# Kernel tuning notes

Hardware: AMD Instinct MI355X
Metric: run time of the kernel (lower is better)

Reference implementation:

```python
import jax, jax.numpy as jnp
import numpy as np

DEPTH = 8  # binary soft-decision-tree depth (n_node = 2**DEPTH - 1, n_leaf = 2**DEPTH)


def setup_inputs() -> dict:
    key = jax.random.key(0)
    k0, k1, k2 = jax.random.split(key, 3)
    B, T, D = 32, 2048, 512
    K, L = 8, 16  # n_trees, n_label
    n_node = 2 ** DEPTH - 1
    n_leaf = 2 ** DEPTH
    x = jax.random.normal(k0, (B, T, D), dtype=jnp.float32)
    W = jax.random.normal(k1, (K, n_node, D), dtype=jnp.float32) * (1.0 / np.sqrt(D))
    b = jnp.zeros((K, n_node), dtype=jnp.float32)
    pi = jax.random.uniform(k2, (K, n_leaf, L), dtype=jnp.float32)
    return {"x": x, "W": W, "b": b, "pi": pi, "conditional": 1, "dependence_length": -1}


def _tree_preds(x, W, b, pi):
    # decision probs for all trees at once: [K, B, T, n_node]
    d = jax.nn.sigmoid(jnp.einsum('btf,knf->kbtn', x, W) + b[:, None, None, :])
    mu = jnp.ones(d.shape[:3] + (1,), dtype=d.dtype)  # routing prob, [K,B,T,1]
    begin = 0
    for layer in range(DEPTH):
        w = 2 ** layer
        dl = d[..., begin:begin + w]  # [K,B,T,w]
        # interleave (mu*d, mu*(1-d)) -> children order matches torch repeat/cat flatten
        mu = jnp.stack([mu * dl, mu * (1.0 - dl)], axis=-1).reshape(d.shape[:3] + (2 * w,))
        begin += w
    # leaf distributions: softmax over labels of pi, then mix by routing probs
    return jnp.einsum('kbtl,kln->kbtn', mu, jax.nn.softmax(pi, axis=-1))  # [K,B,T,L]


def reference(x, W, b, pi, conditional, dependence_length):
    K = W.shape[0]
    L = pi.shape[-1]
    B, T, _ = x.shape
    tp = _tree_preds(x, W, b, pi)  # [K,B,T,L]
    if not conditional:
        return tp.sum(0) * (1.0 / L)
    if dependence_length == -1:
        tp_t = jnp.transpose(tp, (2, 1, 0, 3))  # [T,B,K,L] for token scan
        init = jnp.full((B, L), 1.0 / L, dtype=x.dtype)
        def step(tmp, tpt):
            tmp = jax.lax.stop_gradient(tmp)  # mirrors clone().detach()
            new = jnp.einsum('bkl,bk->bl', tpt, tmp[:, :K])
            return jax.nn.softmax(jnp.exp(new), axis=1), new
        _, preds = jax.lax.scan(step, init, tp_t)  # preds: [T,B,L]
        return jnp.transpose(preds, (1, 0, 2))
    # dependence_length >= 1 path
    pred = tp.sum(0) / K
    pad = jnp.full((B, 1, L), 1.0 / L, dtype=x.dtype)
    for _ in range(1, dependence_length):
        shifted = jnp.concatenate([pad, pred[:, :-1, :]], axis=1)
        pred = jnp.einsum('kbtl,btk->btl', tp, shifted[:, :, :K])
    return pred
```

## Files before the change

### kernel.cpp

```cpp
#include <hip/hip_runtime.h>

#define KT 8
#define NN 255
#define LL 16
#define DD 512
#define BB 32
#define TT 2048
#define MM (BB*TT)

typedef short short8 __attribute__((ext_vector_type(8)));
typedef float floatx4 __attribute__((ext_vector_type(4)));

__device__ __forceinline__ unsigned bf16_rne(float v) {
    unsigned u = __float_as_uint(v);
    return (u + 0x7FFFu + ((u >> 16) & 1u)) >> 16;
}

__device__ __forceinline__ void gll16(const char* g, char* l) {
    __builtin_amdgcn_global_load_lds(
        (const __attribute__((address_space(1))) unsigned int*)g,
        (__attribute__((address_space(3))) unsigned int*)l, 16, 0, 0);
}

__global__ void k_prep_x(const float* __restrict__ x, short* __restrict__ xh,
                         short* __restrict__ xl) {
    size_t g = (size_t)blockIdx.x * 256 + threadIdx.x;
    const float4* xv = (const float4*)x;
    float4 a = xv[g * 2], b = xv[g * 2 + 1];
    float v[8] = {a.x, a.y, a.z, a.w, b.x, b.y, b.z, b.w};
    short8 hh, ll;
    #pragma unroll
    for (int j = 0; j < 8; ++j) {
        unsigned h = bf16_rne(v[j]);
        hh[j] = (short)h;
        ll[j] = (short)bf16_rne(v[j] - __uint_as_float(h << 16));
    }
    ((short8*)xh)[g] = hh;
    ((short8*)xl)[g] = ll;
}

__global__ void k_prep_sp(const float* __restrict__ pi, float* __restrict__ spd) {
    int g = blockIdx.x * blockDim.x + threadIdx.x;
    const float* p = pi + (size_t)g * LL;
    float v[LL];
    float mx = -1e30f;
    #pragma unroll
    for (int l = 0; l < LL; ++l) { v[l] = p[l]; mx = fmaxf(mx, v[l]); }
    float s = 0.f;
    #pragma unroll
    for (int l = 0; l < LL; ++l) { v[l] = __expf(v[l] - mx); s += v[l]; }
    const float inv = 1.0f / s;
    float* o = spd + (size_t)g * LL;
    #pragma unroll
    for (int l = 0; l < LL; ++l) o[l] = v[l] * inv;
}

__global__ void k_prep_b(const float* __restrict__ W, short* __restrict__ Bp) {
    int g = blockIdx.x * 256 + threadIdx.x;
    int lane = g & 63;
    int nt = (g >> 6) & 15;
    int kb = (g >> 10) & 15;
    int kt = g >> 14;
    int n = nt * 16 + (lane & 15);
    int k0 = kb * 32 + ((lane >> 4) << 3);
    short8 hh = {0,0,0,0,0,0,0,0}, ll = {0,0,0,0,0,0,0,0};
    if (n < NN) {
        const float* wp = W + ((size_t)kt * NN + n) * DD + k0;
        floatx4 a = *(const floatx4*)wp;
        floatx4 b = *(const floatx4*)(wp + 4);
        float xv[8] = {a[0], a[1], a[2], a[3], b[0], b[1], b[2], b[3]};
        #pragma unroll
        for (int j = 0; j < 8; ++j) {
            unsigned h = bf16_rne(xv[j]);
            hh[j] = (short)h;
            ll[j] = (short)bf16_rne(xv[j] - __uint_as_float(h << 16));
        }
    }
    size_t base = ((((size_t)kt * 16 + kb) * 16 + nt) * 2) * 64;
    ((short8*)Bp)[base + lane] = hh;
    ((short8*)Bp)[base + 64 + lane] = ll;
}

__global__ void k_prep_spf(const float* __restrict__ spd, short* __restrict__ spf) {
    int g = blockIdx.x * 64 + threadIdx.x;
    int lane = g & 63;
    int ks = (g >> 6) & 7;
    int kt = g >> 9;
    int n = lane & 15;
    int oct = lane >> 4;
    short8 hh, ll;
    #pragma unroll
    for (int j = 0; j < 8; ++j) {
        int leaf = ks * 32 + oct * 8 + j;
        float v = spd[((size_t)kt * 256 + leaf) * 16 + n];
        unsigned h = bf16_rne(v);
        hh[j] = (short)h;
        ll[j] = (short)bf16_rne(v - __uint_as_float(h << 16));
    }
    size_t base = ((size_t)(kt * 8 + ks) * 2) * 64;
    ((short8*)spf)[base + lane] = hh;
    ((short8*)spf)[base + 64 + lane] = ll;
}

__launch_bounds__(512, 2)
__global__ void k_forest(const short* __restrict__ xh, const short* __restrict__ xl,
                         const short* __restrict__ Bp, const float* __restrict__ bias,
                         const short* __restrict__ spf, float* __restrict__ tp) {
    __shared__ __align__(16) char smem[65536];
    const int tid  = threadIdx.x;
    const int lane = tid & 63;
    const int wv   = tid >> 6;
    const int wr   = wv >> 1;
    const int wc   = wv & 1;
    const int kt   = blockIdx.x;
    const int mb   = blockIdx.y;
    const int oct  = lane >> 4;

    const int mrow0 = mb * 128 + wr * 32;
    const short* xhb = xh + (size_t)(mrow0 + (lane & 15)) * DD + (oct << 3);
    const short* xlb = xl + (size_t)(mrow0 + (lane & 15)) * DD + (oct << 3);
    const char* bsrc = (const char*)Bp + (size_t)kt * 16 * 32768;

    float breg[8];
    #pragma unroll
    for (int ntl = 0; ntl < 8; ++ntl) {
        int n = wc * 128 + ntl * 16 + (lane & 15);
        breg[ntl] = (n < NN) ? bias[kt * NN + n] : 0.f;
    }

    floatx4 acc[2][8];
    #pragma unroll
    for (int mt = 0; mt < 2; ++mt)
        #pragma unroll
        for (int ntl = 0; ntl < 8; ++ntl)
            acc[mt][ntl] = (floatx4){0.f, 0.f, 0.f, 0.f};

    short8 ahc[2], alc[2], ahn[2], aln[2];

    #pragma unroll
    for (int i = 0; i < 4; ++i)
        gll16(bsrc + i * 8192 + tid * 16, (char*)smem + i * 8192 + tid * 16);
    #pragma unroll
    for (int mt = 0; mt < 2; ++mt) {
        ahc[mt] = *(const short8*)(xhb + (size_t)mt * 16 * DD);
        alc[mt] = *(const short8*)(xlb + (size_t)mt * 16 * DD);
    }
    __syncthreads();

    #pragma unroll 2
    for (int kb = 0; kb < 16; ++kb) {
        char* cur = (char*)smem + ((kb & 1) ? 32768 : 0);
        char* nxt = (char*)smem + ((kb & 1) ? 0 : 32768);
        if (kb < 15) {
            const char* s = bsrc + (size_t)(kb + 1) * 32768;
            #pragma unroll
            for (int i = 0; i < 4; ++i)
                gll16(s + i * 8192 + tid * 16, nxt + i * 8192 + tid * 16);
            #pragma unroll
            for (int mt = 0; mt < 2; ++mt) {
                ahn[mt] = *(const short8*)(xhb + (size_t)mt * 16 * DD + (kb + 1) * 32);
                aln[mt] = *(const short8*)(xlb + (size_t)mt * 16 * DD + (kb + 1) * 32);
            }
        }
        const short8* bf = (const short8*)cur;
        #pragma unroll
        for (int ntl = 0; ntl < 8; ++ntl) {
            const int nt = wc * 8 + ntl;
            short8 bh = bf[(size_t)(nt * 2 + 0) * 64 + lane];
            short8 bl = bf[(size_t)(nt * 2 + 1) * 64 + lane];
            #pragma unroll
            for (int mt = 0; mt < 2; ++mt) {
                acc[mt][ntl] = __builtin_amdgcn_mfma_f32_16x16x32_bf16(ahc[mt], bh, acc[mt][ntl], 0, 0, 0);
                acc[mt][ntl] = __builtin_amdgcn_mfma_f32_16x16x32_bf16(ahc[mt], bl, acc[mt][ntl], 0, 0, 0);
                acc[mt][ntl] = __builtin_amdgcn_mfma_f32_16x16x32_bf16(alc[mt], bh, acc[mt][ntl], 0, 0, 0);
            }
        }
        __syncthreads();
        #pragma unroll
        for (int mt = 0; mt < 2; ++mt) {
            ahc[mt] = ahn[mt]; alc[mt] = aln[mt];
        }
    }

    float* dls = (float*)smem;
    const short8* spl = (const short8*)((char*)smem + 33280);
    floatx4* ps = (floatx4*)((char*)smem + 49664);

    {
        const floatx4* src = (const floatx4*)(spf + (size_t)kt * 8192);
        floatx4* dst = (floatx4*)((char*)smem + 33280);
        dst[tid] = src[tid];
        dst[512 + tid] = src[512 + tid];
    }

    const int mtile = wv & 1;
    const int wg = wv >> 1;
    const int mloc = mtile * 16 + (lane & 15);

    #pragma unroll 1
    for (int p = 0; p < 4; ++p) {
        __syncthreads();
        if (wr == p) {
            #pragma unroll
            for (int mt = 0; mt < 2; ++mt)
                #pragma unroll
                for (int ntl = 0; ntl < 8; ++ntl)
                    #pragma unroll
                    for (int i = 0; i < 4; ++i) {
                        float lg = acc[mt][ntl][i] + breg[ntl];
                        float dv = 1.f / (1.f + __expf(-lg));
                        int mrow = mt * 16 + oct * 4 + i;
                        int n = wc * 128 + ntl * 16 + (lane & 15);
                        dls[mrow * 260 + n] = dv;
                    }
        }
        __syncthreads();

        const float* dm = dls + mloc * 260;
        floatx4 pacc = (floatx4){0.f, 0.f, 0.f, 0.f};
        #pragma unroll
        for (int kss = 0; kss < 2; ++kss) {
            const int ks = wg * 2 + kss;
            const int leaf0 = ks * 32 + oct * 8;
            float d0 = dm[0];
            float d1 = dm[1 + (leaf0 >> 7)];
            float d2 = dm[3 + (leaf0 >> 6)];
            float d3 = dm[7 + (leaf0 >> 5)];
            float d4 = dm[15 + (leaf0 >> 4)];
            float d5 = dm[31 + (leaf0 >> 3)];
            float n6a = dm[63 + (leaf0 >> 2)];
            float n6b = dm[64 + (leaf0 >> 2)];
            float v70 = dm[127 + (leaf0 >> 1)];
            float v71 = dm[128 + (leaf0 >> 1)];
            float v72 = dm[129 + (leaf0 >> 1)];
            float v73 = dm[130 + (leaf0 >> 1)];
            float P = (((leaf0 >> 7) & 1) ? (1.f - d0) : d0)
                    * (((leaf0 >> 6) & 1) ? (1.f - d1) : d1)
                    * (((leaf0 >> 5) & 1) ? (1.f - d2) : d2)
                    * (((leaf0 >> 4) & 1) ? (1.f - d3) : d3)
                    * (((leaf0 >> 3) & 1) ? (1.f - d4) : d4);
            float pA = P * d5, pB = P * (1.f - d5);
            float q0 = pA * n6a, q1 = pA * (1.f - n6a);
            float q2 = pB * n6b, q3 = pB * (1.f - n6b);
            float mu[8];
            mu[0] = q0 * v70; mu[1] = q0 * (1.f - v70);
            mu[2] = q1 * v71; mu[3] = q1 * (1.f - v71);
            mu[4] = q2 * v72; mu[5] = q2 * (1.f - v72);
            mu[6] = q3 * v73; mu[7] = q3 * (1.f - v73);
            short8 mh, ml;
            #pragma unroll
            for (int j = 0; j < 8; ++j) {
                unsigned h = bf16_rne(mu[j]);
                mh[j] = (short)h;
                ml[j] = (short)bf16_rne(mu[j] - __uint_as_float(h << 16));
            }
            short8 sh = spl[(ks * 2 + 0) * 64 + lane];
            short8 sl = spl[(ks * 2 + 1) * 64 + lane];
            pacc = __builtin_amdgcn_mfma_f32_16x16x32_bf16(mh, sh, pacc, 0, 0, 0);
            pacc = __builtin_amdgcn_mfma_f32_16x16x32_bf16(mh, sl, pacc, 0, 0, 0);
            pacc = __builtin_amdgcn_mfma_f32_16x16x32_bf16(ml, sh, pacc, 0, 0, 0);
        }
        ps[(mtile * 4 + wg) * 64 + lane] = pacc;
        __syncthreads();
        if (wv < 2) {
            const int mt2 = wv;
            floatx4 r = ps[(mt2 * 4 + 0) * 64 + lane] + ps[(mt2 * 4 + 1) * 64 + lane]
                      + ps[(mt2 * 4 + 2) * 64 + lane] + ps[(mt2 * 4 + 3) * 64 + lane];
            #pragma unroll
            for (int i = 0; i < 4; ++i) {
                size_t mg = (size_t)mb * 128 + p * 32 + mt2 * 16 + oct * 4 + i;
                tp[mg * 128 + kt * 16 + (lane & 15)] = r[i];
            }
        }
    }
}

__device__ __forceinline__ float dpp_sum16(float v) {
    int i;
    i = __builtin_amdgcn_update_dpp(0, __float_as_int(v), 0xB1, 0xF, 0xF, true);
    v += __int_as_float(i);
    i = __builtin_amdgcn_update_dpp(0, __float_as_int(v), 0x4E, 0xF, 0xF, true);
    v += __int_as_float(i);
    i = __builtin_amdgcn_update_dpp(0, __float_as_int(v), 0x141, 0xF, 0xF, true);
    v += __int_as_float(i);
    i = __builtin_amdgcn_update_dpp(0, __float_as_int(v), 0x140, 0xF, 0xF, true);
    v += __int_as_float(i);
    return v;
}

__device__ __forceinline__ float rdl(float v, int k) {
    return __int_as_float(__builtin_amdgcn_readlane(__float_as_int(v), k));
}

#define SCAN_STEP(C, t) do { \
    float nw = ((C[0]*w0 + C[1]*w1) + (C[2]*w2 + C[3]*w3)) \
             + ((C[4]*w4 + C[5]*w5) + (C[6]*w6 + C[7]*w7)); \
    nw *= rinv; \
    ob[(size_t)(t) * 16] = nw; \
    float e1 = __expf(nw); \
    float wx = __expf(e1); \
    if ((t) + 8 < TT) { \
        _Pragma("unroll") \
        for (int k = 0; k < 8; ++k) C[k] = base[(size_t)((t) + 8) * 128 + k * 16]; \
    } \
    float ssum = dpp_sum16(wx); \
    rinv = __builtin_amdgcn_rcpf(ssum); \
    w0 = rdl(wx, 0); w1 = rdl(wx, 1); w2 = rdl(wx, 2); w3 = rdl(wx, 3); \
    w4 = rdl(wx, 4); w5 = rdl(wx, 5); w6 = rdl(wx, 6); w7 = rdl(wx, 7); \
} while (0)

__global__ void k_scan(const float* __restrict__ tp, float* __restrict__ out) {
    const int b = blockIdx.x;
    const int l = threadIdx.x;
    if (l >= 16) return;
    const float* base = tp + (size_t)b * TT * 128 + l;
    float* ob = out + (size_t)b * TT * 16 + l;
    float w0 = 1.f, w1 = 1.f, w2 = 1.f, w3 = 1.f, w4 = 1.f, w5 = 1.f, w6 = 1.f, w7 = 1.f;
    float rinv = 1.f / 16.f;
    float c0[8], c1[8], c2[8], c3[8], c4[8], c5[8], c6[8], c7[8];
    #pragma unroll
    for (int k = 0; k < 8; ++k) {
        c0[k] = base[(size_t)0 * 128 + k * 16];
        c1[k] = base[(size_t)1 * 128 + k * 16];
        c2[k] = base[(size_t)2 * 128 + k * 16];
        c3[k] = base[(size_t)3 * 128 + k * 16];
        c4[k] = base[(size_t)4 * 128 + k * 16];
        c5[k] = base[(size_t)5 * 128 + k * 16];
        c6[k] = base[(size_t)6 * 128 + k * 16];
        c7[k] = base[(size_t)7 * 128 + k * 16];
    }
    for (int t0 = 0; t0 < TT; t0 += 8) {
        SCAN_STEP(c0, t0 + 0);
        SCAN_STEP(c1, t0 + 1);
        SCAN_STEP(c2, t0 + 2);
        SCAN_STEP(c3, t0 + 3);
        SCAN_STEP(c4, t0 + 4);
        SCAN_STEP(c5, t0 + 5);
        SCAN_STEP(c6, t0 + 6);
        SCAN_STEP(c7, t0 + 7);
    }
}

extern "C" void kernel_launch(void* const* d_in, const int* in_sizes, int n_in,
                              void* d_out, int out_size, void* d_ws, size_t ws_size,
                              hipStream_t stream) {
    const float* x  = (const float*)d_in[0];
    const float* W  = (const float*)d_in[1];
    const float* b  = (const float*)d_in[2];
    const float* pi = (const float*)d_in[3];
    float* ws = (float*)d_ws;
    float* tp  = ws;
    short* xh  = (short*)(ws + 8388608);
    short* xl  = xh + 33554432;
    short* Bp  = xl + 33554432;
    short* spf = Bp + 2097152;
    float* spd = (float*)(spf + 65536);
    float* out = (float*)d_out;

    k_prep_x<<<dim3(16384), dim3(256), 0, stream>>>(x, xh, xl);
    k_prep_sp<<<dim3(8), dim3(256), 0, stream>>>(pi, spd);
    k_prep_b<<<dim3(512), dim3(256), 0, stream>>>(W, Bp);
    k_prep_spf<<<dim3(64), dim3(64), 0, stream>>>(spd, spf);
    k_forest<<<dim3(8, 512), dim3(512), 0, stream>>>(xh, xl, Bp, b, spf, tp);
    k_scan<<<dim3(BB), dim3(64), 0, stream>>>(tp, out);
}
```

Before: 1.300 ms.

## Retile forest GEMM waves, transpose scan input layout, fuse leaf-softmax prep kernels

Several changes land together. The forest GEMM switches its wave grid from 4x2 to 2x4, so each wave owns a 64x64 tile and reuses each B fragment across four M tiles instead of two. The tree-prediction buffer is stored label-major with trees contiguous, padded per batch, so the serial scan reads each step with two float4 loads instead of eight strided scalar loads. The scan also normalises the weights before broadcasting them and drops the tail guard by relying on the padding. The two softmax/bf16-split prep kernels are merged into one that uses shared memory, removing a launch and an intermediate buffer. The larger accumulator footprint raises register pressure.

```diff
diff --git a/kernel.cpp b/kernel.cpp
--- a/kernel.cpp
+++ b/kernel.cpp
@@ -7,6 +7,7 @@
 #define BB 32
 #define TT 2048
 #define MM (BB*TT)
+#define TPS_STRIDE (2056*128)
 
 typedef short short8 __attribute__((ext_vector_type(8)));
 typedef float floatx4 __attribute__((ext_vector_type(4)));
@@ -39,9 +40,11 @@
     ((short8*)xl)[g] = ll;
 }
 
-__global__ void k_prep_sp(const float* __restrict__ pi, float* __restrict__ spd) {
-    int g = blockIdx.x * blockDim.x + threadIdx.x;
-    const float* p = pi + (size_t)g * LL;
+__global__ void k_prep_sp(const float* __restrict__ pi, short* __restrict__ spf) {
+    __shared__ float sm[256 * 16];
+    const int kt = blockIdx.x;
+    const int tid = threadIdx.x;
+    const float* p = pi + ((size_t)kt * 256 + tid) * LL;
     float v[LL];
     float mx = -1e30f;
     #pragma unroll
@@ -50,9 +53,27 @@
     #pragma unroll
     for (int l = 0; l < LL; ++l) { v[l] = __expf(v[l] - mx); s += v[l]; }
     const float inv = 1.0f / s;
-    float* o = spd + (size_t)g * LL;
-    #pragma unroll
-    for (int l = 0; l < LL; ++l) o[l] = v[l] * inv;
+    #pragma unroll
+    for (int l = 0; l < LL; ++l) sm[tid * 16 + l] = v[l] * inv;
+    __syncthreads();
+    #pragma unroll
+    for (int it = 0; it < 2; ++it) {
+        int item = it * 256 + tid;
+        int ks = item >> 6, lane = item & 63;
+        int n = lane & 15, oct = lane >> 4;
+        short8 hh, ll;
+        #pragma unroll
+        for (int j = 0; j < 8; ++j) {
+            int leaf = ks * 32 + oct * 8 + j;
+            float val = sm[leaf * 16 + n];
+            unsigned h = bf16_rne(val);
+            hh[j] = (short)h;
+            ll[j] = (short)bf16_rne(val - __uint_as_float(h << 16));
+        }
+        size_t base = ((size_t)(kt * 8 + ks) * 2) * 64;
+        ((short8*)spf)[base + lane] = hh;
+        ((short8*)spf)[base + 64 + lane] = ll;
+    }
 }
 
 __global__ void k_prep_b(const float* __restrict__ W, short* __restrict__ Bp) {
@@ -81,67 +102,46 @@
     ((short8*)Bp)[base + 64 + lane] = ll;
 }
 
-__global__ void k_prep_spf(const float* __restrict__ spd, short* __restrict__ spf) {
-    int g = blockIdx.x * 64 + threadIdx.x;
-    int lane = g & 63;
-    int ks = (g >> 6) & 7;
-    int kt = g >> 9;
-    int n = lane & 15;
-    int oct = lane >> 4;
-    short8 hh, ll;
-    #pragma unroll
-    for (int j = 0; j < 8; ++j) {
-        int leaf = ks * 32 + oct * 8 + j;
-        float v = spd[((size_t)kt * 256 + leaf) * 16 + n];
-        unsigned h = bf16_rne(v);
-        hh[j] = (short)h;
-        ll[j] = (short)bf16_rne(v - __uint_as_float(h << 16));
-    }
-    size_t base = ((size_t)(kt * 8 + ks) * 2) * 64;
-    ((short8*)spf)[base + lane] = hh;
-    ((short8*)spf)[base + 64 + lane] = ll;
-}
-
 __launch_bounds__(512, 2)
 __global__ void k_forest(const short* __restrict__ xh, const short* __restrict__ xl,
                          const short* __restrict__ Bp, const float* __restrict__ bias,
-                         const short* __restrict__ spf, float* __restrict__ tp) {
+                         const short* __restrict__ spf, float* __restrict__ tps) {
     __shared__ __align__(16) char smem[65536];
     const int tid  = threadIdx.x;
     const int lane = tid & 63;
     const int wv   = tid >> 6;
-    const int wr   = wv >> 1;
-    const int wc   = wv & 1;
+    const int wr   = wv >> 2;
+    const int wc   = wv & 3;
     const int kt   = blockIdx.x;
     const int mb   = blockIdx.y;
     const int oct  = lane >> 4;
-
-    const int mrow0 = mb * 128 + wr * 32;
-    const short* xhb = xh + (size_t)(mrow0 + (lane & 15)) * DD + (oct << 3);
-    const short* xlb = xl + (size_t)(mrow0 + (lane & 15)) * DD + (oct << 3);
+    const int lr   = lane & 15;
+
+    const short* xhb = xh + (size_t)(mb * 128 + wr * 64 + lr) * DD + (oct << 3);
+    const short* xlb = xl + (size_t)(mb * 128 + wr * 64 + lr) * DD + (oct << 3);
     const char* bsrc = (const char*)Bp + (size_t)kt * 16 * 32768;
 
-    float breg[8];
-    #pragma unroll
-    for (int ntl = 0; ntl < 8; ++ntl) {
-        int n = wc * 128 + ntl * 16 + (lane & 15);
+    float breg[4];
+    #pragma unroll
+    for (int ntl = 0; ntl < 4; ++ntl) {
+        int n = (wc * 4 + ntl) * 16 + lr;
         breg[ntl] = (n < NN) ? bias[kt * NN + n] : 0.f;
     }
 
-    floatx4 acc[2][8];
-    #pragma unroll
-    for (int mt = 0; mt < 2; ++mt)
-        #pragma unroll
-        for (int ntl = 0; ntl < 8; ++ntl)
+    floatx4 acc[4][4];
+    #pragma unroll
+    for (int mt = 0; mt < 4; ++mt)
+        #pragma unroll
+        for (int ntl = 0; ntl < 4; ++ntl)
             acc[mt][ntl] = (floatx4){0.f, 0.f, 0.f, 0.f};
 
-    short8 ahc[2], alc[2], ahn[2], aln[2];
+    short8 ahc[4], alc[4], ahn[4], aln[4];
 
     #pragma unroll
     for (int i = 0; i < 4; ++i)
         gll16(bsrc + i * 8192 + tid * 16, (char*)smem + i * 8192 + tid * 16);
     #pragma unroll
-    for (int mt = 0; mt < 2; ++mt) {
+    for (int mt = 0; mt < 4; ++mt) {
         ahc[mt] = *(const short8*)(xhb + (size_t)mt * 16 * DD);
         alc[mt] = *(const short8*)(xlb + (size_t)mt * 16 * DD);
     }
@@ -157,19 +157,19 @@
             for (int i = 0; i < 4; ++i)
                 gll16(s + i * 8192 + tid * 16, nxt + i * 8192 + tid * 16);
             #pragma unroll
-            for (int mt = 0; mt < 2; ++mt) {
+            for (int mt = 0; mt < 4; ++mt) {
                 ahn[mt] = *(const short8*)(xhb + (size_t)mt * 16 * DD + (kb + 1) * 32);
                 aln[mt] = *(const short8*)(xlb + (size_t)mt * 16 * DD + (kb + 1) * 32);
             }
         }
         const short8* bf = (const short8*)cur;
         #pragma unroll
-        for (int ntl = 0; ntl < 8; ++ntl) {
-            const int nt = wc * 8 + ntl;
+        for (int ntl = 0; ntl < 4; ++ntl) {
+            const int nt = wc * 4 + ntl;
             short8 bh = bf[(size_t)(nt * 2 + 0) * 64 + lane];
             short8 bl = bf[(size_t)(nt * 2 + 1) * 64 + lane];
             #pragma unroll
-            for (int mt = 0; mt < 2; ++mt) {
+            for (int mt = 0; mt < 4; ++mt) {
                 acc[mt][ntl] = __builtin_amdgcn_mfma_f32_16x16x32_bf16(ahc[mt], bh, acc[mt][ntl], 0, 0, 0);
                 acc[mt][ntl] = __builtin_amdgcn_mfma_f32_16x16x32_bf16(ahc[mt], bl, acc[mt][ntl], 0, 0, 0);
                 acc[mt][ntl] = __builtin_amdgcn_mfma_f32_16x16x32_bf16(alc[mt], bh, acc[mt][ntl], 0, 0, 0);
@@ -177,7 +177,7 @@
         }
         __syncthreads();
         #pragma unroll
-        for (int mt = 0; mt < 2; ++mt) {
+        for (int mt = 0; mt < 4; ++mt) {
             ahc[mt] = ahn[mt]; alc[mt] = aln[mt];
         }
     }
@@ -195,22 +195,23 @@
 
     const int mtile = wv & 1;
     const int wg = wv >> 1;
-    const int mloc = mtile * 16 + (lane & 15);
+    const int mloc = mtile * 16 + lr;
 
     #pragma unroll 1
     for (int p = 0; p < 4; ++p) {
         __syncthreads();
-        if (wr == p) {
-            #pragma unroll
-            for (int mt = 0; mt < 2; ++mt)
+        if (wr == (p >> 1)) {
+            const int mts = (p & 1) * 2;
+            #pragma unroll
+            for (int mtl = 0; mtl < 2; ++mtl)
                 #pragma unroll
-                for (int ntl = 0; ntl < 8; ++ntl)
+                for (int ntl = 0; ntl < 4; ++ntl)
                     #pragma unroll
                     for (int i = 0; i < 4; ++i) {
-                        float lg = acc[mt][ntl][i] + breg[ntl];
+                        float lg = acc[mts + mtl][ntl][i] + breg[ntl];
                         float dv = 1.f / (1.f + __expf(-lg));
-                        int mrow = mt * 16 + oct * 4 + i;
-                        int n = wc * 128 + ntl * 16 + (lane & 15);
+                        int mrow = mtl * 16 + oct * 4 + i;
+                        int n = (wc * 4 + ntl) * 16 + lr;
                         dls[mrow * 260 + n] = dv;
                     }
         }
@@ -268,8 +269,9 @@
                       + ps[(mt2 * 4 + 2) * 64 + lane] + ps[(mt2 * 4 + 3) * 64 + lane];
             #pragma unroll
             for (int i = 0; i < 4; ++i) {
-                size_t mg = (size_t)mb * 128 + p * 32 + mt2 * 16 + oct * 4 + i;
-                tp[mg * 128 + kt * 16 + (lane & 15)] = r[i];
+                int mg = mb * 128 + p * 32 + mt2 * 16 + oct * 4 + i;
+                int bb_ = mg >> 11, t = mg & 2047;
+                tps[(size_t)bb_ * TPS_STRIDE + (size_t)t * 128 + lr * 8 + kt] = r[i];
             }
         }
     }
@@ -292,52 +294,46 @@
     return __int_as_float(__builtin_amdgcn_readlane(__float_as_int(v), k));
 }
 
-#define SCAN_STEP(C, t) do { \
-    float nw = ((C[0]*w0 + C[1]*w1) + (C[2]*w2 + C[3]*w3)) \
-             + ((C[4]*w4 + C[5]*w5) + (C[6]*w6 + C[7]*w7)); \
-    nw *= rinv; \
+#define SCAN_STEP(CA, CB, t) do { \
+    float nw = ((CA[0]*w0 + CA[1]*w1) + (CA[2]*w2 + CA[3]*w3)) \
+             + ((CB[0]*w4 + CB[1]*w5) + (CB[2]*w6 + CB[3]*w7)); \
     ob[(size_t)(t) * 16] = nw; \
-    float e1 = __expf(nw); \
-    float wx = __expf(e1); \
-    if ((t) + 8 < TT) { \
-        _Pragma("unroll") \
-        for (int k = 0; k < 8; ++k) C[k] = base[(size_t)((t) + 8) * 128 + k * 16]; \
-    } \
+    float wx = __expf(__expf(nw)); \
+    CA = *(const floatx4*)(base + (size_t)((t) + 8) * 128); \
+    CB = *(const floatx4*)(base + (size_t)((t) + 8) * 128 + 4); \
     float ssum = dpp_sum16(wx); \
-    rinv = __builtin_amdgcn_rcpf(ssum); \
-    w0 = rdl(wx, 0); w1 = rdl(wx, 1); w2 = rdl(wx, 2); w3 = rdl(wx, 3); \
-    w4 = rdl(wx, 4); w5 = rdl(wx, 5); w6 = rdl(wx, 6); w7 = rdl(wx, 7); \
+    float wn = wx * __builtin_amdgcn_rcpf(ssum); \
+    w0 = rdl(wn, 0); w1 = rdl(wn, 1); w2 = rdl(wn, 2); w3 = rdl(wn, 3); \
+    w4 = rdl(wn, 4); w5 = rdl(wn, 5); w6 = rdl(wn, 6); w7 = rdl(wn, 7); \
 } while (0)
 
-__global__ void k_scan(const float* __restrict__ tp, float* __restrict__ out) {
+__global__ void k_scan(const float* __restrict__ tps, float* __restrict__ out) {
     const int b = blockIdx.x;
     const int l = threadIdx.x;
     if (l >= 16) return;
-    const float* base = tp + (size_t)b * TT * 128 + l;
+    const float* base = tps + (size_t)b * TPS_STRIDE + l * 8;
     float* ob = out + (size_t)b * TT * 16 + l;
-    float w0 = 1.f, w1 = 1.f, w2 = 1.f, w3 = 1.f, w4 = 1.f, w5 = 1.f, w6 = 1.f, w7 = 1.f;
-    float rinv = 1.f / 16.f;
-    float c0[8], c1[8], c2[8], c3[8], c4[8], c5[8], c6[8], c7[8];
-    #pragma unroll
-    for (int k = 0; k < 8; ++k) {
-        c0[k] = base[(size_t)0 * 128 + k * 16];
-        c1[k] = base[(size_t)1 * 128 + k * 16];
-        c2[k] = base[(size_t)2 * 128 + k * 16];
-        c3[k] = base[(size_t)3 * 128 + k * 16];
-        c4[k] = base[(size_t)4 * 128 + k * 16];
-        c5[k] = base[(size_t)5 * 128 + k * 16];
-        c6[k] = base[(size_t)6 * 128 + k * 16];
-        c7[k] = base[(size_t)7 * 128 + k * 16];
-    }
+    float w0 = 1.f/16.f, w1 = 1.f/16.f, w2 = 1.f/16.f, w3 = 1.f/16.f;
+    float w4 = 1.f/16.f, w5 = 1.f/16.f, w6 = 1.f/16.f, w7 = 1.f/16.f;
+    floatx4 a0, a1, a2, a3, a4, a5, a6, a7;
+    floatx4 b0, b1, b2, b3, b4, b5, b6, b7;
+    a0 = *(const floatx4*)(base + 0*128); b0 = *(const floatx4*)(base + 0*128 + 4);
+    a1 = *(const floatx4*)(base + 1*128); b1 = *(const floatx4*)(base + 1*128 + 4);
+    a2 = *(const floatx4*)(base + 2*128); b2 = *(const floatx4*)(base + 2*128 + 4);
+    a3 = *(const floatx4*)(base + 3*128); b3 = *(const floatx4*)(base + 3*128 + 4);
+    a4 = *(const floatx4*)(base + 4*128); b4 = *(const floatx4*)(base + 4*128 + 4);
+    a5 = *(const floatx4*)(base + 5*128); b5 = *(const floatx4*)(base + 5*128 + 4);
+    a6 = *(const floatx4*)(base + 6*128); b6 = *(const floatx4*)(base + 6*128 + 4);
+    a7 = *(const floatx4*)(base + 7*128); b7 = *(const floatx4*)(base + 7*128 + 4);
     for (int t0 = 0; t0 < TT; t0 += 8) {
-        SCAN_STEP(c0, t0 + 0);
-        SCAN_STEP(c1, t0 + 1);
-        SCAN_STEP(c2, t0 + 2);
-        SCAN_STEP(c3, t0 + 3);
-        SCAN_STEP(c4, t0 + 4);
-        SCAN_STEP(c5, t0 + 5);
-        SCAN_STEP(c6, t0 + 6);
-        SCAN_STEP(c7, t0 + 7);
+        SCAN_STEP(a0, b0, t0 + 0);
+        SCAN_STEP(a1, b1, t0 + 1);
+        SCAN_STEP(a2, b2, t0 + 2);
+        SCAN_STEP(a3, b3, t0 + 3);
+        SCAN_STEP(a4, b4, t0 + 4);
+        SCAN_STEP(a5, b5, t0 + 5);
+        SCAN_STEP(a6, b6, t0 + 6);
+        SCAN_STEP(a7, b7, t0 + 7);
     }
 }
 
@@ -349,18 +345,16 @@
     const float* b  = (const float*)d_in[2];
     const float* pi = (const float*)d_in[3];
     float* ws = (float*)d_ws;
-    float* tp  = ws;
-    short* xh  = (short*)(ws + 8388608);
+    float* tps = ws;
+    short* xh  = (short*)(ws + 8421376);
     short* xl  = xh + 33554432;
     short* Bp  = xl + 33554432;
     short* spf = Bp + 2097152;
-    float* spd = (float*)(spf + 65536);
     float* out = (float*)d_out;
 
     k_prep_x<<<dim3(16384), dim3(256), 0, stream>>>(x, xh, xl);
-    k_prep_sp<<<dim3(8), dim3(256), 0, stream>>>(pi, spd);
+    k_prep_sp<<<dim3(8), dim3(256), 0, stream>>>(pi, spf);
     k_prep_b<<<dim3(512), dim3(256), 0, stream>>>(W, Bp);
-    k_prep_spf<<<dim3(64), dim3(64), 0, stream>>>(spd, spf);
-    k_forest<<<dim3(8, 512), dim3(512), 0, stream>>>(xh, xl, Bp, b, spf, tp);
-    k_scan<<<dim3(BB), dim3(64), 0, stream>>>(tp, out);
-}
+    k_forest<<<dim3(8, 512), dim3(512), 0, stream>>>(xh, xl, Bp, b, spf, tps);
+    k_scan<<<dim3(BB), dim3(64), 0, stream>>>(tps, out);
+}
```

Measured after the change: 2.403 ms. +84.9%, slower.
